# Kernel tuning notes

Hardware: AMD Instinct MI355X
Metric: run time of the kernel (lower is better)

## Reference

```python
import jax, jax.numpy as jnp
import numpy as np

B, I, O, G = 262144, 3, 64, 128


def setup_inputs() -> dict:
    key = jax.random.key(0)
    kx, kc = jax.random.split(key)
    x = jax.random.uniform(kx, (1, B, I), dtype=jnp.float32)  # coords in [0,1)
    coeffs = jax.random.normal(kc, (2, O, I, G), dtype=jnp.float32) / (
        np.float32(np.sqrt(I) * np.sqrt(G))
    )
    bias = jnp.zeros((1, O), dtype=jnp.float32)
    return {"x": x, "coeffs": coeffs, "bias": bias}


def reference(x, coeffs, bias):
    # x: (1, B, I); coeffs: (2, O, I, G); bias: (1, O)
    b, i = x.shape[1], x.shape[2]
    two, o, _, g = coeffs.shape
    k = jnp.arange(1, g + 1, dtype=x.dtype)          # (G,)
    kx = x.reshape(b, i, 1) * k                      # (B, I, G)
    cosf = jnp.cos(kx).reshape(b, i * g)             # (B, I*G)
    sinf = jnp.sin(kx).reshape(b, i * g)             # (B, I*G)
    w = coeffs.reshape(2, o, i * g)                  # (2, O, I*G)
    # sum over (input_dim, gridsize) fused as one GEMM per trig branch
    out = cosf @ w[0].T + sinf @ w[1].T + bias       # (B, O)
    return out
```

## Files before the change

kernel.cpp:

```cpp
#include <hip/hip_runtime.h>
#include <hip/hip_bf16.h>

typedef __attribute__((ext_vector_type(8))) short short8;
typedef __attribute__((ext_vector_type(4))) float f32x4;
typedef __attribute__((ext_vector_type(2))) float f32x2;

#define NROWS   262144
#define ODIM    64
#define KSTEPS  24
#define NBLOCKS 256
#define TPB     1024
#define INV2PI  0.15915494309189535f

__device__ __forceinline__ float cos2pi(float f){ float r; asm("v_cos_f32 %0, %1" : "=v"(r) : "v"(f)); return r; }
__device__ __forceinline__ float sin2pi(float f){ float r; asm("v_sin_f32 %0, %1" : "=v"(r) : "v"(f)); return r; }

__device__ __forceinline__ short bf16_of(float f){
    union { __hip_bfloat16 h; short s; } u;
    u.h = __float2bfloat16(f);
    return u.s;
}

extern "C" __global__ void __launch_bounds__(TPB, 4)
fourier_mfma(const float* __restrict__ x,
             const float* __restrict__ coeffs,
             const float* __restrict__ bias,
             float* __restrict__ out)
{
    __shared__ short8 Wlds[KSTEPS * 4 * 64];

    const int tid = threadIdx.x;

    for (int fl = tid; fl < KSTEPS*4*64; fl += TPB) {
        const int ks = fl >> 8;
        const int nt = (fl >> 6) & 3;
        const int ln = fl & 63;
        const int o  = nt*16 + (ln & 15);
        const int kg = ln >> 4;
        union { short8 v; short s[8]; } fr;
        #pragma unroll
        for (int h = 0; h < 2; ++h) {
            const int kb  = ks*32 + h*16;
            const int br  = (kb >= 384) ? 1 : 0;
            const int rem = kb - br*384;
            const int ii  = rem >> 7;
            const int g0  = (rem & 127) + kg*4;
            const float* wp = coeffs + (((br*ODIM + o)*3 + ii) << 7) + g0;
            #pragma unroll
            for (int j = 0; j < 4; ++j) fr.s[h*4 + j] = bf16_of(wp[j]);
        }
        Wlds[fl] = fr.v;
    }
    __syncthreads();

    const int lane = tid & 63;
    const int wid  = tid >> 6;
    const int mrow = lane & 15;
    const int kgrp = lane >> 4;
    const float hs = (float)(4*kgrp + 1);

    float bcol[4];
    #pragma unroll
    for (int nt = 0; nt < 4; ++nt) bcol[nt] = bias[nt*16 + mrow];

    const int unit = blockIdx.x * 16 + wid;
    const int base = unit * 64;

    for (int rg = 0; rg < 2; ++rg) {
        const int rowA = base + (rg*2 + 0)*16 + mrow;
        const int rowB = base + (rg*2 + 1)*16 + mrow;

        f32x2 xr[3];
        #pragma unroll
        for (int i = 0; i < 3; ++i)
            xr[i] = (f32x2){ x[rowA*3 + i] * INV2PI, x[rowB*3 + i] * INV2PI };

        f32x4 acc[2][4];
        #pragma unroll
        for (int rr = 0; rr < 2; ++rr)
            #pragma unroll
            for (int nt = 0; nt < 4; ++nt)
                acc[rr][nt] = (f32x4){0.f, 0.f, 0.f, 0.f};

        f32x2 cvp, svp, c16p, s16p, stc, sts;

        #pragma unroll
        for (int kk = 0; kk < 12; ++kk) {
            short8 bfr[8];
            #pragma unroll
            for (int nt = 0; nt < 4; ++nt) {
                bfr[nt]     = Wlds[(kk*4 + nt)*64 + lane];
                bfr[4 + nt] = Wlds[((kk + 12)*4 + nt)*64 + lane];
            }

            if ((kk & 3) == 0) {
                const int i = kk >> 2;
                const f32x2 a = xr[i];
                cvp = (f32x2){ cos2pi(a.x), cos2pi(a.y) };
                svp = (f32x2){ sin2pi(a.x), sin2pi(a.y) };
                f32x2 t = (f32x2){ 16.f*a.x, 16.f*a.y };
                t.x -= floorf(t.x); t.y -= floorf(t.y);
                c16p = (f32x2){ cos2pi(t.x), cos2pi(t.y) };
                s16p = (f32x2){ sin2pi(t.x), sin2pi(t.y) };
                f32x2 u = (f32x2){ hs*a.x, hs*a.y };
                u.x -= floorf(u.x); u.y -= floorf(u.y);
                stc = (f32x2){ cos2pi(u.x), cos2pi(u.y) };
                sts = (f32x2){ sin2pi(u.x), sin2pi(u.y) };
            }

            union { short8 v; short s[8]; } fc[2], fs[2];
            #pragma unroll
            for (int h = 0; h < 2; ++h) {
                f32x2 c = stc, s = sts;
                fc[0].s[h*4] = bf16_of(c.x); fc[1].s[h*4] = bf16_of(c.y);
                fs[0].s[h*4] = bf16_of(s.x); fs[1].s[h*4] = bf16_of(s.y);
                #pragma unroll
                for (int j = 1; j < 4; ++j) {
                    const f32x2 cn = c*cvp - s*svp;
                    const f32x2 sn = s*cvp + c*svp;
                    c = cn; s = sn;
                    fc[0].s[h*4+j] = bf16_of(c.x); fc[1].s[h*4+j] = bf16_of(c.y);
                    fs[0].s[h*4+j] = bf16_of(s.x); fs[1].s[h*4+j] = bf16_of(s.y);
                }
                const f32x2 nc = stc*c16p - sts*s16p;
                const f32x2 ns = sts*c16p + stc*s16p;
                stc = nc; sts = ns;
            }

            #pragma unroll
            for (int nt = 0; nt < 4; ++nt) {
                #pragma unroll
                for (int rr = 0; rr < 2; ++rr) {
                    acc[rr][nt] = __builtin_amdgcn_mfma_f32_16x16x32_bf16(fc[rr].v, bfr[nt],     acc[rr][nt], 0, 0, 0);
                    acc[rr][nt] = __builtin_amdgcn_mfma_f32_16x16x32_bf16(fs[rr].v, bfr[4 + nt], acc[rr][nt], 0, 0, 0);
                }
            }
        }

        #pragma unroll
        for (int rr = 0; rr < 2; ++rr) {
            const int row0 = base + (rg*2 + rr)*16 + kgrp*4;
            #pragma unroll
            for (int nt = 0; nt < 4; ++nt) {
                #pragma unroll
                for (int q = 0; q < 4; ++q) {
                    out[(row0 + q)*ODIM + nt*16 + mrow] = acc[rr][nt][q] + bcol[nt];
                }
            }
        }
    }
}

extern "C" void kernel_launch(void* const* d_in, const int* in_sizes, int n_in,
                              void* d_out, int out_size, void* d_ws, size_t ws_size,
                              hipStream_t stream) {
    const float* x      = (const float*)d_in[0];
    const float* coeffs = (const float*)d_in[1];
    const float* bias   = (const float*)d_in[2];
    float* out = (float*)d_out;
    (void)in_sizes; (void)n_in; (void)out_size; (void)d_ws; (void)ws_size;
    hipLaunchKernelGGL(fourier_mfma, dim3(NBLOCKS), dim3(TPB), 0, stream, x, coeffs, bias, out);
}
```

Measured before the change: 41.85 us.

## Switch to 32x32x16 bf16 MFMA tiles and process all 64 rows per wave

Replaces the 16x16x32 MFMA tiling with 32x32x16 tiles. Each wave now handles its 64 rows in a single pass as two 32-row tiles against two 32-column tiles, instead of two passes over 16-row tiles. The LDS weight layout is reshaped to match, so each lane loads 8 contiguous bf16 weights. Each lane generates 8 consecutive harmonics by angle-addition recurrence, which roughly halves the number of B-fragment loads and recurrence-reset steps per MFMA. It also raises instruction priority around the MFMA group. The cost is that the 32x32 accumulators (64 floats per lane) raise register pressure, and the longer 8-step recurrence may lose some precision.

```diff
diff --git a/kernel.cpp b/kernel.cpp
--- a/kernel.cpp
+++ b/kernel.cpp
@@ -1,13 +1,12 @@
 #include <hip/hip_runtime.h>
 #include <hip/hip_bf16.h>
 
-typedef __attribute__((ext_vector_type(8))) short short8;
-typedef __attribute__((ext_vector_type(4))) float f32x4;
-typedef __attribute__((ext_vector_type(2))) float f32x2;
+typedef __attribute__((ext_vector_type(8)))  short short8;
+typedef __attribute__((ext_vector_type(16))) float f32x16;
+typedef __attribute__((ext_vector_type(2)))  float f32x2;
 
 #define NROWS   262144
 #define ODIM    64
-#define KSTEPS  24
 #define NBLOCKS 256
 #define TPB     1024
 #define INV2PI  0.15915494309189535f
@@ -27,125 +26,116 @@
              const float* __restrict__ bias,
              float* __restrict__ out)
 {
-    __shared__ short8 Wlds[KSTEPS * 4 * 64];
+    __shared__ short8 Wlds[24*2*2*64];
 
     const int tid = threadIdx.x;
 
-    for (int fl = tid; fl < KSTEPS*4*64; fl += TPB) {
-        const int ks = fl >> 8;
-        const int nt = (fl >> 6) & 3;
+    for (int fl = tid; fl < 24*2*2*64; fl += TPB) {
         const int ln = fl & 63;
-        const int o  = nt*16 + (ln & 15);
-        const int kg = ln >> 4;
+        const int ct = (fl >> 6) & 1;
+        const int br = (fl >> 7) & 1;
+        const int pk = fl >> 8;
+        const int o   = ct*32 + (ln & 31);
+        const int rem = pk*16 + (ln >> 5)*8;
+        const int ii  = rem >> 7;
+        const int g0  = rem & 127;
+        const float* wp = coeffs + (((br*ODIM + o)*3 + ii) << 7) + g0;
         union { short8 v; short s[8]; } fr;
         #pragma unroll
-        for (int h = 0; h < 2; ++h) {
-            const int kb  = ks*32 + h*16;
-            const int br  = (kb >= 384) ? 1 : 0;
-            const int rem = kb - br*384;
-            const int ii  = rem >> 7;
-            const int g0  = (rem & 127) + kg*4;
-            const float* wp = coeffs + (((br*ODIM + o)*3 + ii) << 7) + g0;
-            #pragma unroll
-            for (int j = 0; j < 4; ++j) fr.s[h*4 + j] = bf16_of(wp[j]);
-        }
+        for (int j = 0; j < 8; ++j) fr.s[j] = bf16_of(wp[j]);
         Wlds[fl] = fr.v;
     }
     __syncthreads();
 
     const int lane = tid & 63;
     const int wid  = tid >> 6;
-    const int mrow = lane & 15;
-    const int kgrp = lane >> 4;
-    const float hs = (float)(4*kgrp + 1);
-
-    float bcol[4];
-    #pragma unroll
-    for (int nt = 0; nt < 4; ++nt) bcol[nt] = bias[nt*16 + mrow];
+    const int col  = lane & 31;
+    const int half = lane >> 5;
 
     const int unit = blockIdx.x * 16 + wid;
     const int base = unit * 64;
+    const int rowA = base + col;
+    const int rowB = base + 32 + col;
 
-    for (int rg = 0; rg < 2; ++rg) {
-        const int rowA = base + (rg*2 + 0)*16 + mrow;
-        const int rowB = base + (rg*2 + 1)*16 + mrow;
+    f32x2 xr[3];
+    #pragma unroll
+    for (int i = 0; i < 3; ++i)
+        xr[i] = (f32x2){ x[rowA*3 + i] * INV2PI, x[rowB*3 + i] * INV2PI };
 
-        f32x2 xr[3];
+    const float bias0 = bias[col];
+    const float bias1 = bias[32 + col];
+
+    f32x16 acc[2][2];
+    #pragma unroll
+    for (int rt = 0; rt < 2; ++rt)
         #pragma unroll
-        for (int i = 0; i < 3; ++i)
-            xr[i] = (f32x2){ x[rowA*3 + i] * INV2PI, x[rowB*3 + i] * INV2PI };
+        for (int ct = 0; ct < 2; ++ct)
+            #pragma unroll
+            for (int q = 0; q < 16; ++q) acc[rt][ct][q] = 0.f;
 
-        f32x4 acc[2][4];
-        #pragma unroll
-        for (int rr = 0; rr < 2; ++rr)
-            #pragma unroll
-            for (int nt = 0; nt < 4; ++nt)
-                acc[rr][nt] = (f32x4){0.f, 0.f, 0.f, 0.f};
+    f32x2 cv, sv, c16, s16, stc, sts;
+    const float h0f = (float)(half*8 + 1);
 
-        f32x2 cvp, svp, c16p, s16p, stc, sts;
+    #pragma unroll
+    for (int pk = 0; pk < 24; ++pk) {
+        const short8 b00 = Wlds[pk*256 +   0 +  0 + lane];
+        const short8 b01 = Wlds[pk*256 +   0 + 64 + lane];
+        const short8 b10 = Wlds[pk*256 + 128 +  0 + lane];
+        const short8 b11 = Wlds[pk*256 + 128 + 64 + lane];
 
-        #pragma unroll
-        for (int kk = 0; kk < 12; ++kk) {
-            short8 bfr[8];
-            #pragma unroll
-            for (int nt = 0; nt < 4; ++nt) {
-                bfr[nt]     = Wlds[(kk*4 + nt)*64 + lane];
-                bfr[4 + nt] = Wlds[((kk + 12)*4 + nt)*64 + lane];
-            }
-
-            if ((kk & 3) == 0) {
-                const int i = kk >> 2;
-                const f32x2 a = xr[i];
-                cvp = (f32x2){ cos2pi(a.x), cos2pi(a.y) };
-                svp = (f32x2){ sin2pi(a.x), sin2pi(a.y) };
-                f32x2 t = (f32x2){ 16.f*a.x, 16.f*a.y };
-                t.x -= floorf(t.x); t.y -= floorf(t.y);
-                c16p = (f32x2){ cos2pi(t.x), cos2pi(t.y) };
-                s16p = (f32x2){ sin2pi(t.x), sin2pi(t.y) };
-                f32x2 u = (f32x2){ hs*a.x, hs*a.y };
-                u.x -= floorf(u.x); u.y -= floorf(u.y);
-                stc = (f32x2){ cos2pi(u.x), cos2pi(u.y) };
-                sts = (f32x2){ sin2pi(u.x), sin2pi(u.y) };
-            }
-
-            union { short8 v; short s[8]; } fc[2], fs[2];
-            #pragma unroll
-            for (int h = 0; h < 2; ++h) {
-                f32x2 c = stc, s = sts;
-                fc[0].s[h*4] = bf16_of(c.x); fc[1].s[h*4] = bf16_of(c.y);
-                fs[0].s[h*4] = bf16_of(s.x); fs[1].s[h*4] = bf16_of(s.y);
-                #pragma unroll
-                for (int j = 1; j < 4; ++j) {
-                    const f32x2 cn = c*cvp - s*svp;
-                    const f32x2 sn = s*cvp + c*svp;
-                    c = cn; s = sn;
-                    fc[0].s[h*4+j] = bf16_of(c.x); fc[1].s[h*4+j] = bf16_of(c.y);
-                    fs[0].s[h*4+j] = bf16_of(s.x); fs[1].s[h*4+j] = bf16_of(s.y);
-                }
-                const f32x2 nc = stc*c16p - sts*s16p;
-                const f32x2 ns = sts*c16p + stc*s16p;
-                stc = nc; sts = ns;
-            }
-
-            #pragma unroll
-            for (int nt = 0; nt < 4; ++nt) {
-                #pragma unroll
-                for (int rr = 0; rr < 2; ++rr) {
-                    acc[rr][nt] = __builtin_amdgcn_mfma_f32_16x16x32_bf16(fc[rr].v, bfr[nt],     acc[rr][nt], 0, 0, 0);
-                    acc[rr][nt] = __builtin_amdgcn_mfma_f32_16x16x32_bf16(fs[rr].v, bfr[4 + nt], acc[rr][nt], 0, 0, 0);
-                }
-            }
+        if ((pk & 7) == 0) {
+            const f32x2 a = xr[pk >> 3];
+            cv = (f32x2){ cos2pi(a.x), cos2pi(a.y) };
+            sv = (f32x2){ sin2pi(a.x), sin2pi(a.y) };
+            f32x2 t = (f32x2){ 16.f*a.x, 16.f*a.y };
+            t.x -= floorf(t.x); t.y -= floorf(t.y);
+            c16 = (f32x2){ cos2pi(t.x), cos2pi(t.y) };
+            s16 = (f32x2){ sin2pi(t.x), sin2pi(t.y) };
+            f32x2 u = (f32x2){ h0f*a.x, h0f*a.y };
+            u.x -= floorf(u.x); u.y -= floorf(u.y);
+            stc = (f32x2){ cos2pi(u.x), cos2pi(u.y) };
+            sts = (f32x2){ sin2pi(u.x), sin2pi(u.y) };
         }
 
+        union { short8 v; short s[8]; } fAc, fAs, fBc, fBs;
+        {
+            f32x2 c = stc, s = sts;
+            fAc.s[0] = bf16_of(c.x); fBc.s[0] = bf16_of(c.y);
+            fAs.s[0] = bf16_of(s.x); fBs.s[0] = bf16_of(s.y);
+            #pragma unroll
+            for (int j = 1; j < 8; ++j) {
+                const f32x2 cn = c*cv - s*sv;
+                const f32x2 sn = s*cv + c*sv;
+                c = cn; s = sn;
+                fAc.s[j] = bf16_of(c.x); fBc.s[j] = bf16_of(c.y);
+                fAs.s[j] = bf16_of(s.x); fBs.s[j] = bf16_of(s.y);
+            }
+            const f32x2 nc = stc*c16 - sts*s16;
+            const f32x2 ns = sts*c16 + stc*s16;
+            stc = nc; sts = ns;
+        }
+
+        __builtin_amdgcn_s_setprio(1);
+        acc[0][0] = __builtin_amdgcn_mfma_f32_32x32x16_bf16(fAc.v, b00, acc[0][0], 0, 0, 0);
+        acc[0][1] = __builtin_amdgcn_mfma_f32_32x32x16_bf16(fAc.v, b01, acc[0][1], 0, 0, 0);
+        acc[1][0] = __builtin_amdgcn_mfma_f32_32x32x16_bf16(fBc.v, b00, acc[1][0], 0, 0, 0);
+        acc[1][1] = __builtin_amdgcn_mfma_f32_32x32x16_bf16(fBc.v, b01, acc[1][1], 0, 0, 0);
+        acc[0][0] = __builtin_amdgcn_mfma_f32_32x32x16_bf16(fAs.v, b10, acc[0][0], 0, 0, 0);
+        acc[0][1] = __builtin_amdgcn_mfma_f32_32x32x16_bf16(fAs.v, b11, acc[0][1], 0, 0, 0);
+        acc[1][0] = __builtin_amdgcn_mfma_f32_32x32x16_bf16(fBs.v, b10, acc[1][0], 0, 0, 0);
+        acc[1][1] = __builtin_amdgcn_mfma_f32_32x32x16_bf16(fBs.v, b11, acc[1][1], 0, 0, 0);
+        __builtin_amdgcn_s_setprio(0);
+    }
+
+    #pragma unroll
+    for (int rt = 0; rt < 2; ++rt) {
         #pragma unroll
-        for (int rr = 0; rr < 2; ++rr) {
-            const int row0 = base + (rg*2 + rr)*16 + kgrp*4;
+        for (int ct = 0; ct < 2; ++ct) {
+            const float bv = ct ? bias1 : bias0;
             #pragma unroll
-            for (int nt = 0; nt < 4; ++nt) {
-                #pragma unroll
-                for (int q = 0; q < 4; ++q) {
-                    out[(row0 + q)*ODIM + nt*16 + mrow] = acc[rr][nt][q] + bcol[nt];
-                }
+            for (int q = 0; q < 16; ++q) {
+                const int row = base + rt*32 + (q & 3) + 8*(q >> 2) + 4*half;
+                out[row*ODIM + ct*32 + col] = acc[rt][ct][q] + bv;
             }
         }
     }
```

Result: slower. 102.3 us (+144.4%).

## Software-pipeline trig feature generation with MFMA and pack bf16 pairs

Applied to the files above, without the earlier changes.

Computes the bf16 cos/sin fragments for the next k-step while issuing MFMAs for the current one, using a double-buffered register array. Converts pairs of floats with the packed v_cvt_pk_bf16_f32 instruction instead of per-element conversions. Also hoists the x loads above the barrier so they overlap the LDS weight staging, and raises wave priority around the MFMA block. This adds register pressure from the double buffer and a fully unrolled outer loop, which could hurt occupancy.

```diff
diff --git a/kernel.cpp b/kernel.cpp
--- a/kernel.cpp
+++ b/kernel.cpp
@@ -4,21 +4,22 @@
 typedef __attribute__((ext_vector_type(8))) short short8;
 typedef __attribute__((ext_vector_type(4))) float f32x4;
 typedef __attribute__((ext_vector_type(2))) float f32x2;
+typedef __attribute__((ext_vector_type(4))) unsigned int u32x4;
 
 #define NROWS   262144
 #define ODIM    64
-#define KSTEPS  24
 #define NBLOCKS 256
 #define TPB     1024
 #define INV2PI  0.15915494309189535f
 
 __device__ __forceinline__ float cos2pi(float f){ float r; asm("v_cos_f32 %0, %1" : "=v"(r) : "v"(f)); return r; }
 __device__ __forceinline__ float sin2pi(float f){ float r; asm("v_sin_f32 %0, %1" : "=v"(r) : "v"(f)); return r; }
-
+__device__ __forceinline__ unsigned pkbf(float lo, float hi){
+    unsigned r; asm("v_cvt_pk_bf16_f32 %0, %1, %2" : "=v"(r) : "v"(lo), "v"(hi)); return r;
+}
+__device__ __forceinline__ short8 as_s8(u32x4 v){ union{u32x4 u; short8 s;} x; x.u = v; return x.s; }
 __device__ __forceinline__ short bf16_of(float f){
-    union { __hip_bfloat16 h; short s; } u;
-    u.h = __float2bfloat16(f);
-    return u.s;
+    union { __hip_bfloat16 h; short s; } u; u.h = __float2bfloat16(f); return u.s;
 }
 
 extern "C" __global__ void __launch_bounds__(TPB, 4)
@@ -27,11 +28,11 @@
              const float* __restrict__ bias,
              float* __restrict__ out)
 {
-    __shared__ short8 Wlds[KSTEPS * 4 * 64];
+    __shared__ short8 Wlds[24 * 4 * 64];
 
     const int tid = threadIdx.x;
 
-    for (int fl = tid; fl < KSTEPS*4*64; fl += TPB) {
+    for (int fl = tid; fl < 24*4*64; fl += TPB) {
         const int ks = fl >> 8;
         const int nt = (fl >> 6) & 3;
         const int ln = fl & 63;
@@ -51,30 +52,66 @@
         }
         Wlds[fl] = fr.v;
     }
-    __syncthreads();
 
     const int lane = tid & 63;
     const int wid  = tid >> 6;
     const int mrow = lane & 15;
     const int kgrp = lane >> 4;
-    const float hs = (float)(4*kgrp + 1);
+    const float h0f = (float)(4*kgrp + 1);
 
+    const int unit = blockIdx.x * 16 + wid;
+    const int base = unit * 64;
+
+    f32x2 xr[2][3];
+    #pragma unroll
+    for (int rg = 0; rg < 2; ++rg) {
+        const int rowA = base + (rg*2 + 0)*16 + mrow;
+        const int rowB = base + (rg*2 + 1)*16 + mrow;
+        #pragma unroll
+        for (int i = 0; i < 3; ++i)
+            xr[rg][i] = (f32x2){ x[rowA*3 + i] * INV2PI, x[rowB*3 + i] * INV2PI };
+    }
     float bcol[4];
     #pragma unroll
     for (int nt = 0; nt < 4; ++nt) bcol[nt] = bias[nt*16 + mrow];
 
-    const int unit = blockIdx.x * 16 + wid;
-    const int base = unit * 64;
+    __syncthreads();
 
+#define ANCHOR(RG, I) do {                                          \
+    const f32x2 a = xr[RG][I];                                      \
+    cv  = (f32x2){ cos2pi(a.x), cos2pi(a.y) };                      \
+    sv  = (f32x2){ sin2pi(a.x), sin2pi(a.y) };                      \
+    f32x2 t = (f32x2){ 16.f*a.x, 16.f*a.y };                        \
+    t.x -= floorf(t.x); t.y -= floorf(t.y);                         \
+    c16 = (f32x2){ cos2pi(t.x), cos2pi(t.y) };                      \
+    s16 = (f32x2){ sin2pi(t.x), sin2pi(t.y) };                      \
+    f32x2 u = (f32x2){ h0f*a.x, h0f*a.y };                          \
+    u.x -= floorf(u.x); u.y -= floorf(u.y);                         \
+    stc = (f32x2){ cos2pi(u.x), cos2pi(u.y) };                      \
+    sts = (f32x2){ sin2pi(u.x), sin2pi(u.y) };                      \
+} while (0)
+
+#define HALF(D0, D1, FCA, FCB, FSA, FSB) do {                       \
+    const f32x2 c0 = stc,        s0 = sts;                          \
+    const f32x2 c1 = c0*cv - s0*sv, s1 = s0*cv + c0*sv;             \
+    FCA.D0 = pkbf(c0.x, c1.x);  FCB.D0 = pkbf(c0.y, c1.y);          \
+    FSA.D0 = pkbf(s0.x, s1.x);  FSB.D0 = pkbf(s0.y, s1.y);          \
+    const f32x2 c2 = c1*cv - s1*sv, s2 = s1*cv + c1*sv;             \
+    const f32x2 c3 = c2*cv - s2*sv, s3 = s2*cv + c2*sv;             \
+    FCA.D1 = pkbf(c2.x, c3.x);  FCB.D1 = pkbf(c2.y, c3.y);          \
+    FSA.D1 = pkbf(s2.x, s3.x);  FSB.D1 = pkbf(s2.y, s3.y);          \
+    const f32x2 nc = stc*c16 - sts*s16, ns = sts*c16 + stc*s16;     \
+    stc = nc; sts = ns;                                             \
+} while (0)
+
+#define FEAT(RG, KKP, FCA, FCB, FSA, FSB) do {                      \
+    if (((KKP) & 3) == 0) ANCHOR(RG, (KKP) >> 2);                   \
+    HALF(x, y, FCA, FCB, FSA, FSB);                                 \
+    HALF(z, w, FCA, FCB, FSA, FSB);                                 \
+} while (0)
+
+    #pragma unroll
     for (int rg = 0; rg < 2; ++rg) {
-        const int rowA = base + (rg*2 + 0)*16 + mrow;
-        const int rowB = base + (rg*2 + 1)*16 + mrow;
-
-        f32x2 xr[3];
-        #pragma unroll
-        for (int i = 0; i < 3; ++i)
-            xr[i] = (f32x2){ x[rowA*3 + i] * INV2PI, x[rowB*3 + i] * INV2PI };
-
         f32x4 acc[2][4];
         #pragma unroll
         for (int rr = 0; rr < 2; ++rr)
@@ -82,59 +119,38 @@
             for (int nt = 0; nt < 4; ++nt)
                 acc[rr][nt] = (f32x4){0.f, 0.f, 0.f, 0.f};
 
-        f32x2 cvp, svp, c16p, s16p, stc, sts;
+        f32x2 cv, sv, c16, s16, stc, sts;
+        u32x4 F[2][4];
+
+        FEAT(rg, 0, F[0][0], F[0][1], F[0][2], F[0][3]);
 
         #pragma unroll
         for (int kk = 0; kk < 12; ++kk) {
-            short8 bfr[8];
+            const int cb = kk & 1;
+            short8 bc[4], bs[4];
             #pragma unroll
             for (int nt = 0; nt < 4; ++nt) {
-                bfr[nt]     = Wlds[(kk*4 + nt)*64 + lane];
-                bfr[4 + nt] = Wlds[((kk + 12)*4 + nt)*64 + lane];
+                bc[nt] = Wlds[(kk*4 + nt)*64 + lane];
+                bs[nt] = Wlds[((kk + 12)*4 + nt)*64 + lane];
             }
 
-            if ((kk & 3) == 0) {
-                const int i = kk >> 2;
-                const f32x2 a = xr[i];
-                cvp = (f32x2){ cos2pi(a.x), cos2pi(a.y) };
-                svp = (f32x2){ sin2pi(a.x), sin2pi(a.y) };
-                f32x2 t = (f32x2){ 16.f*a.x, 16.f*a.y };
-                t.x -= floorf(t.x); t.y -= floorf(t.y);
-                c16p = (f32x2){ cos2pi(t.x), cos2pi(t.y) };
-                s16p = (f32x2){ sin2pi(t.x), sin2pi(t.y) };
-                f32x2 u = (f32x2){ hs*a.x, hs*a.y };
-                u.x -= floorf(u.x); u.y -= floorf(u.y);
-                stc = (f32x2){ cos2pi(u.x), cos2pi(u.y) };
-                sts = (f32x2){ sin2pi(u.x), sin2pi(u.y) };
-            }
+            if (kk < 11)
+                FEAT(rg, kk+1, F[cb^1][0], F[cb^1][1], F[cb^1][2], F[cb^1][3]);
 
-            union { short8 v; short s[8]; } fc[2], fs[2];
-            #pragma unroll
-            for (int h = 0; h < 2; ++h) {
-                f32x2 c = stc, s = sts;
-                fc[0].s[h*4] = bf16_of(c.x); fc[1].s[h*4] = bf16_of(c.y);
-                fs[0].s[h*4] = bf16_of(s.x); fs[1].s[h*4] = bf16_of(s.y);
-                #pragma unroll
-                for (int j = 1; j < 4; ++j) {
-                    const f32x2 cn = c*cvp - s*svp;
-                    const f32x2 sn = s*cvp + c*svp;
-                    c = cn; s = sn;
-                    fc[0].s[h*4+j] = bf16_of(c.x); fc[1].s[h*4+j] = bf16_of(c.y);
-                    fs[0].s[h*4+j] = bf16_of(s.x); fs[1].s[h*4+j] = bf16_of(s.y);
-                }
-                const f32x2 nc = stc*c16p - sts*s16p;
-                const f32x2 ns = sts*c16p + stc*s16p;
-                stc = nc; sts = ns;
-            }
+            const short8 fAc = as_s8(F[cb][0]);
+            const short8 fBc = as_s8(F[cb][1]);
+            const short8 fAs = as_s8(F[cb][2]);
+            const short8 fBs = as_s8(F[cb][3]);
 
+            __builtin_amdgcn_s_setprio(1);
             #pragma unroll
             for (int nt = 0; nt < 4; ++nt) {
-                #pragma unroll
-                for (int rr = 0; rr < 2; ++rr) {
-                    acc[rr][nt] = __builtin_amdgcn_mfma_f32_16x16x32_bf16(fc[rr].v, bfr[nt],     acc[rr][nt], 0, 0, 0);
-                    acc[rr][nt] = __builtin_amdgcn_mfma_f32_16x16x32_bf16(fs[rr].v, bfr[4 + nt], acc[rr][nt], 0, 0, 0);
-                }
+                acc[0][nt] = __builtin_amdgcn_mfma_f32_16x16x32_bf16(fAc, bc[nt], acc[0][nt], 0, 0, 0);
+                acc[1][nt] = __builtin_amdgcn_mfma_f32_16x16x32_bf16(fBc, bc[nt], acc[1][nt], 0, 0, 0);
+                acc[0][nt] = __builtin_amdgcn_mfma_f32_16x16x32_bf16(fAs, bs[nt], acc[0][nt], 0, 0, 0);
+                acc[1][nt] = __builtin_amdgcn_mfma_f32_16x16x32_bf16(fBs, bs[nt], acc[1][nt], 0, 0, 0);
             }
+            __builtin_amdgcn_s_setprio(0);
         }
 
         #pragma unroll
@@ -149,6 +165,9 @@
             }
         }
     }
+#undef FEAT
+#undef HALF
+#undef ANCHOR
 }
 
 extern "C" void kernel_launch(void* const* d_in, const int* in_sizes, int n_in,
```

Result: no change. 41.89 us (+0.1%).
